# Kernel tuning notes

Measured on AMD Instinct MI355X. Metric: run time of the kernel, lower is better.

The kernel has to match this reference:

```python
import jax, jax.numpy as jnp
import numpy as np

DIM = 2048
NUM_HEADS = 16
NUM_KV_HEADS = 4
HEAD_DIM = DIM // NUM_HEADS  # 128


def apply_rotary_emb(x, freqs_cis):
    # x: [b, s, h, head_dim]; freqs_cis: [s, head_dim//2, 2]
    b, s, h, d = x.shape
    xs = x.reshape(b, s, h, d // 2, 2)
    fc = freqs_cis.reshape(1, s, 1, d // 2, 2)
    real = xs[..., 0] * fc[..., 0] - xs[..., 1] * fc[..., 1]
    imag = xs[..., 1] * fc[..., 0] + xs[..., 0] * fc[..., 1]
    return jnp.stack([real, imag], axis=-1).reshape(b, s, h, d)


def setup_inputs() -> dict:
    key = jax.random.key(0)
    k1, k2, k3, k4 = jax.random.split(key, 4)
    b, s = 2, 2048
    x = jax.random.normal(k1, (b, s, DIM), dtype=jnp.float32)
    freqs_cis = jax.random.uniform(k2, (s, HEAD_DIM // 2, 2), dtype=jnp.float32)
    total_kv_dim = (NUM_HEADS + 2 * NUM_KV_HEADS) * HEAD_DIM  # 3072
    wqkv = jax.random.normal(k3, (total_kv_dim, DIM), dtype=jnp.float32) * (DIM ** -0.5)
    wo = jax.random.normal(k4, (DIM, DIM), dtype=jnp.float32) * (DIM ** -0.5)
    return {"x": x, "freqs_cis": freqs_cis, "wqkv": wqkv, "wo": wo}


def reference(x, freqs_cis, wqkv, wo):
    b, s, _ = x.shape
    kv_size = NUM_KV_HEADS * HEAD_DIM
    qkv = jnp.einsum('bsd,od->bso', x, wqkv)
    xq = qkv[..., :DIM].reshape(b, s, NUM_HEADS, HEAD_DIM)
    xk = qkv[..., DIM:DIM + kv_size].reshape(b, s, NUM_KV_HEADS, HEAD_DIM)
    xv = qkv[..., DIM + kv_size:].reshape(b, s, NUM_KV_HEADS, HEAD_DIM)
    xq = apply_rotary_emb(xq, freqs_cis)
    xk = apply_rotary_emb(xk, freqs_cis)
    # -> [b, h, s, d]
    q = xq.transpose(0, 2, 1, 3)
    k = xk.transpose(0, 2, 1, 3)
    v = xv.transpose(0, 2, 1, 3)
    rep = NUM_HEADS // NUM_KV_HEADS
    k = jnp.repeat(k, rep, axis=1)
    v = jnp.repeat(v, rep, axis=1)
    scale = HEAD_DIM ** -0.5
    scores = jnp.einsum('bhqd,bhkd->bhqk', q, k) * scale
    causal = jnp.tril(jnp.ones((s, s), dtype=bool))
    scores = jnp.where(causal[None, None], scores, jnp.finfo(scores.dtype).min)
    attn = jax.nn.softmax(scores, axis=-1)
    out = jnp.einsum('bhqk,bhkd->bhqd', attn, v)
    out = out.transpose(0, 2, 1, 3).reshape(b, s, DIM)
    return jnp.einsum('bsd,od->bso', out, wo)
```

## Files before the change

kernel.cpp:

```cpp
#include <hip/hip_runtime.h>
#include <stdint.h>

typedef uint16_t u16;
typedef float f32x4 __attribute__((ext_vector_type(4)));
typedef short bf16x8 __attribute__((ext_vector_type(8)));

constexpr int NB = 2, NS = 2048, ND = 2048, NH = 16, NKVH = 4, HDIM = 128;
constexpr int QKVD = 3072;
constexpr int TOK = NB * NS;
constexpr float SM_SCALE = 0.08838834764831845f;
constexpr float LOG2E = 1.4426950408889634f;
constexpr float QK_SCALE = SM_SCALE * LOG2E;

#define WAITVM(N) asm volatile("s_waitcnt vmcnt(" #N ")" ::: "memory")
#define WAITLGKM0 asm volatile("s_waitcnt lgkmcnt(0)" ::: "memory")
#define MEMFENCE asm volatile("" ::: "memory")

__device__ __forceinline__ u16 f2bf(float f) {
  union { float f; uint32_t u; } v; v.f = f;
  return (u16)((v.u + 0x7fffu + ((v.u >> 16) & 1u)) >> 16);
}
__device__ __forceinline__ float bf2f(u16 h) {
  union { uint32_t u; float f; } v; v.u = ((uint32_t)h) << 16; return v.f;
}
__device__ __forceinline__ uint32_t cvt_pk_bf16(float lo, float hi) {
  uint32_t r;
  asm("v_cvt_pk_bf16_f32 %0, %1, %2" : "=v"(r) : "v"(lo), "v"(hi));
  return r;
}

__device__ __forceinline__ void gload_lds16(const void* g, void* l) {
  void* gv = const_cast<void*>(g);
  __builtin_amdgcn_global_load_lds(
      (__attribute__((address_space(1))) void*)gv,
      (__attribute__((address_space(3))) void*)l, 16, 0, 0);
}

__global__ __launch_bounds__(256) void cvt_bf16(const float* __restrict__ src,
                                                u16* __restrict__ dst, int n4) {
  int i = blockIdx.x * 256 + threadIdx.x;
  if (i >= n4) return;
  const float4 v = reinterpret_cast<const float4*>(src)[i];
  union { u16 h[4]; uint2 u; } o;
  o.h[0] = f2bf(v.x); o.h[1] = f2bf(v.y); o.h[2] = f2bf(v.z); o.h[3] = f2bf(v.w);
  reinterpret_cast<uint2*>(dst)[i] = o.u;
}

template <int OUTBF>
__global__ __launch_bounds__(256, 2)
void gemm_bt(const u16* __restrict__ A, const u16* __restrict__ Bm,
             void* __restrict__ Cv, int M, int N, int K) {
  __shared__ u16 As[2][128 * 32];
  __shared__ u16 Bs[2][128 * 32];
  const int tid = threadIdx.x;
  const int lane = tid & 63;
  const int wid = tid >> 6;
  const int wr = wid >> 1, wc = wid & 1;
  const int rowA0 = blockIdx.y * 128, colB0 = blockIdx.x * 128;
  const int lr = lane & 15;
  const int lk = (lane >> 4) * 8;
  const char* Ab = (const char*)A;
  const char* Bb = (const char*)Bm;
  f32x4 acc[4][4] = {};
  const int nkt = K >> 5;

  auto STAGE = [&](int kt, int buf) {
#pragma unroll
    for (int p = 0; p < 2; ++p) {
      int o = p * 4096 + tid * 16;
      int row = o >> 6, kb = o & 63;
      gload_lds16(Ab + ((size_t)(rowA0 + row) * K + kt * 32) * 2 + kb, (char*)As[buf] + o);
      gload_lds16(Bb + ((size_t)(colB0 + row) * K + kt * 32) * 2 + kb, (char*)Bs[buf] + o);
    }
  };

  STAGE(0, 0);
  for (int kt = 0; kt < nkt; ++kt) {
    const int cur = kt & 1;
    if (kt + 1 < nkt) { STAGE(kt + 1, cur ^ 1); WAITVM(4); }
    else              { WAITVM(0); }
    __builtin_amdgcn_s_barrier();
    MEMFENCE;
    const u16* Ac = As[cur];
    const u16* Bc = Bs[cur];
    bf16x8 af[4], bfr[4];
#pragma unroll
    for (int m = 0; m < 4; ++m)
      af[m] = *(const bf16x8*)&Ac[(wr * 64 + m * 16 + lr) * 32 + lk];
#pragma unroll
    for (int n = 0; n < 4; ++n)
      bfr[n] = *(const bf16x8*)&Bc[(wc * 64 + n * 16 + lr) * 32 + lk];
    __builtin_amdgcn_s_setprio(1);
#pragma unroll
    for (int m = 0; m < 4; ++m)
#pragma unroll
      for (int n = 0; n < 4; ++n)
        acc[m][n] = __builtin_amdgcn_mfma_f32_16x16x32_bf16(af[m], bfr[n], acc[m][n], 0, 0, 0);
    __builtin_amdgcn_s_setprio(0);
    WAITLGKM0;
    __builtin_amdgcn_s_barrier();
    MEMFENCE;
  }
#pragma unroll
  for (int m = 0; m < 4; ++m) {
    int row0 = rowA0 + wr * 64 + m * 16 + (lane >> 4) * 4;
#pragma unroll
    for (int n = 0; n < 4; ++n) {
      int col = colB0 + wc * 64 + n * 16 + lr;
#pragma unroll
      for (int r = 0; r < 4; ++r) {
        if (OUTBF)
          ((u16*)Cv)[(size_t)(row0 + r) * N + col] = f2bf(acc[m][n][r]);
        else
          ((float*)Cv)[(size_t)(row0 + r) * N + col] = acc[m][n][r];
      }
    }
  }
}

__global__ __launch_bounds__(256)
void rope_split(const u16* __restrict__ qkv, const float* __restrict__ fc,
                u16* __restrict__ Qb, u16* __restrict__ Kb, u16* __restrict__ Vt) {
  const int tok = blockIdx.x;
  const int b = tok >> 11, s = tok & 2047;
  const int tid = threadIdx.x;
  const u16* base = qkv + (size_t)tok * QKVD;
  for (int pp = tid; pp < 1024; pp += 256) {
    int h = pp >> 6, p = pp & 63;
    float x0 = bf2f(base[h * 128 + 2 * p]);
    float x1 = bf2f(base[h * 128 + 2 * p + 1]);
    float c = fc[(s * 64 + p) * 2];
    float sn = fc[(s * 64 + p) * 2 + 1];
    size_t o = ((size_t)(b * NH + h) * NS + s) * HDIM + 2 * p;
    Qb[o] = f2bf(x0 * c - x1 * sn);
    Qb[o + 1] = f2bf(x1 * c + x0 * sn);
  }
  for (int pp = tid; pp < 256; pp += 256) {
    int kv = pp >> 6, p = pp & 63;
    float x0 = bf2f(base[ND + kv * 128 + 2 * p]);
    float x1 = bf2f(base[ND + kv * 128 + 2 * p + 1]);
    float c = fc[(s * 64 + p) * 2];
    float sn = fc[(s * 64 + p) * 2 + 1];
    size_t o = ((size_t)(b * NKVH + kv) * NS + s) * HDIM + 2 * p;
    Kb[o] = f2bf((x0 * c - x1 * sn) * QK_SCALE);
    Kb[o + 1] = f2bf((x1 * c + x0 * sn) * QK_SCALE);
  }
  for (int i = tid; i < 512; i += 256) {
    int kv = i >> 7, d = i & 127;
    float v = bf2f(base[ND + NKVH * HDIM + kv * 128 + d]);
    Vt[((size_t)(b * NKVH + kv) * HDIM + d) * NS + s] = f2bf(v);
  }
}

__global__ __launch_bounds__(512, 2)
void flash_attn(const u16* __restrict__ Qb, const u16* __restrict__ Kb,
                const u16* __restrict__ Vt, u16* __restrict__ Ob) {
  __shared__ u16 Ks[2][64 * 128];
  __shared__ u16 Vs[2][128 * 64];
  const int idx = blockIdx.x;
  const int grp = idx & 7;
  const int b = grp >> 2, kvh = grp & 3;
  const int rest = idx >> 3;
  const int h = kvh * 4 + (rest & 3);
  const int qt = (NS / 128 - 1) - (rest >> 2);
  const int tid = threadIdx.x, lane = tid & 63, w = tid >> 6;
  const int lr = lane & 15, lg = lane >> 4;

  bf16x8 aq[4];
  {
    const u16* Qrow = Qb + ((size_t)(b * NH + h) * NS + qt * 128 + w * 16 + lr) * HDIM;
#pragma unroll
    for (int ks = 0; ks < 4; ++ks)
      aq[ks] = *(const bf16x8*)(Qrow + ks * 32 + lg * 8);
  }
  bf16x8 ones;
#pragma unroll
  for (int j = 0; j < 8; ++j) ones[j] = (short)0x3F80;

  float mrun = -1e30f;
  f32x4 accl = {0.f, 0.f, 0.f, 0.f};
  f32x4 acco[8] = {};

  const char* Kbase = (const char*)(Kb + (size_t)(b * NKVH + kvh) * NS * HDIM);
  const char* Vbase = (const char*)(Vt + (size_t)(b * NKVH + kvh) * HDIM * NS);
  const int qglob = qt * 128 + w * 16 + lr;
  const int qrow0 = qt * 128 + w * 16 + lg * 4;
  const int wave_min_row = qt * 128 + w * 16;
  const int wave_max_row = wave_min_row + 15;

  auto STAGE = [&](int kt, int buf) {
#pragma unroll
    for (int p = 0; p < 2; ++p) {
      int o = p * 8192 + tid * 16;
      int krow = o >> 8, kwb = o & 255;
      gload_lds16(Kbase + (size_t)(kt * 64 + krow) * 256 + (kwb ^ ((krow & 7) << 4)),
                  (char*)Ks[buf] + o);
      int vrow = o >> 7, vwb = o & 127;
      gload_lds16(Vbase + (size_t)vrow * (NS * 2) + kt * 128 + (vwb ^ ((vrow & 7) << 4)),
                  (char*)Vs[buf] + o);
    }
  };

  const int ktmax = 2 * qt + 1;
  STAGE(0, 0);
  for (int kt = 0; kt <= ktmax; ++kt) {
    const int cur = kt & 1;
    if (kt < ktmax) { STAGE(kt + 1, cur ^ 1); WAITVM(4); }
    else            { WAITVM(0); }
    __builtin_amdgcn_s_barrier();
    MEMFENCE;

    if (kt * 64 <= wave_max_row) {
      const char* Kc = (const char*)Ks[cur];
      const char* Vc = (const char*)Vs[cur];

      f32x4 accs[4] = {};
      __builtin_amdgcn_s_setprio(1);
#pragma unroll
      for (int n = 0; n < 4; ++n) {
        int row = n * 16 + lr;
        int swz = (row & 7) << 4;
#pragma unroll
        for (int ks = 0; ks < 4; ++ks) {
          int cb = (ks * 32 + lg * 8) * 2;
          bf16x8 bk = *(const bf16x8*)(Kc + row * 256 + (cb ^ swz));
          accs[n] = __builtin_amdgcn_mfma_f32_16x16x32_bf16(bk, aq[ks], accs[n], 0, 0, 0);
        }
      }
      __builtin_amdgcn_s_setprio(0);

      if (kt * 64 + 63 > wave_min_row) {
#pragma unroll
        for (int n = 0; n < 4; ++n) {
          int kbase = kt * 64 + n * 16 + lg * 4;
#pragma unroll
          for (int r = 0; r < 4; ++r)
            if (kbase + r > qglob) accs[n][r] = -1e30f;
        }
      }

      float pmax = fmaxf(fmaxf(fmaxf(accs[0][0], accs[0][1]), fmaxf(accs[0][2], accs[0][3])),
                         fmaxf(fmaxf(accs[1][0], accs[1][1]), fmaxf(accs[1][2], accs[1][3])));
      pmax = fmaxf(pmax,
             fmaxf(fmaxf(fmaxf(accs[2][0], accs[2][1]), fmaxf(accs[2][2], accs[2][3])),
                   fmaxf(fmaxf(accs[3][0], accs[3][1]), fmaxf(accs[3][2], accs[3][3]))));
      pmax = fmaxf(pmax, __shfl_xor(pmax, 16, 64));
      pmax = fmaxf(pmax, __shfl_xor(pmax, 32, 64));

      bool ok = (pmax <= mrun + 8.f);
      if (!__all(ok)) {
        float mnew = fmaxf(mrun, pmax);
        float alpha = exp2f(mrun - mnew);
        mrun = mnew;
        float alr[4];
#pragma unroll
        for (int r = 0; r < 4; ++r)
          alr[r] = __shfl(alpha, lg * 4 + r, 64);
#pragma unroll
        for (int r = 0; r < 4; ++r) accl[r] *= alr[r];
#pragma unroll
        for (int n2 = 0; n2 < 8; ++n2)
#pragma unroll
          for (int r = 0; r < 4; ++r) acco[n2][r] *= alr[r];
      }

      uint32_t w0[4], w1[4];
#pragma unroll
      for (int n = 0; n < 4; ++n) {
        float p0 = exp2f(accs[n][0] - mrun);
        float p1 = exp2f(accs[n][1] - mrun);
        float p2 = exp2f(accs[n][2] - mrun);
        float p3 = exp2f(accs[n][3] - mrun);
        w0[n] = cvt_pk_bf16(p0, p1);
        w1[n] = cvt_pk_bf16(p2, p3);
      }

      const int s1 = ((lg & 1) << 5) | lr;
      const int s2 = s1 + 16;
      uint32_t F[4][4];
#pragma unroll
      for (int n = 0; n < 4; ++n) {
        F[n][0] = __shfl((int)w0[n], s1, 64);
        F[n][1] = __shfl((int)w1[n], s1, 64);
        F[n][2] = __shfl((int)w0[n], s2, 64);
        F[n][3] = __shfl((int)w1[n], s2, 64);
      }
      const bool hi = (lg & 2);
      bf16x8 pa[2];
#pragma unroll
      for (int ks = 0; ks < 2; ++ks) {
        union { uint32_t d[4]; bf16x8 v; } u;
#pragma unroll
        for (int j = 0; j < 4; ++j)
          u.d[j] = hi ? F[ks * 2 + 1][j] : F[ks * 2][j];
        pa[ks] = u.v;
      }

      __builtin_amdgcn_s_setprio(1);
#pragma unroll
      for (int ks = 0; ks < 2; ++ks) {
        int cb = (ks * 32 + lg * 8) * 2;
#pragma unroll
        for (int n2 = 0; n2 < 8; ++n2) {
          int d = n2 * 16 + lr;
          bf16x8 bv = *(const bf16x8*)(Vc + d * 128 + (cb ^ ((d & 7) << 4)));
          acco[n2] = __builtin_amdgcn_mfma_f32_16x16x32_bf16(pa[ks], bv, acco[n2], 0, 0, 0);
        }
        accl = __builtin_amdgcn_mfma_f32_16x16x32_bf16(pa[ks], ones, accl, 0, 0, 0);
      }
      __builtin_amdgcn_s_setprio(0);
    }
    WAITLGKM0;
    __builtin_amdgcn_s_barrier();
    MEMFENCE;
  }

#pragma unroll
  for (int n2 = 0; n2 < 8; ++n2) {
    int d = n2 * 16 + lr;
#pragma unroll
    for (int r = 0; r < 4; ++r) {
      int q = qrow0 + r;
      Ob[((size_t)b * NS + q) * ND + h * HDIM + d] = f2bf(acco[n2][r] / accl[r]);
    }
  }
}

extern "C" void kernel_launch(void* const* d_in, const int* in_sizes, int n_in,
                              void* d_out, int out_size, void* d_ws, size_t ws_size,
                              hipStream_t stream) {
  const float* x = (const float*)d_in[0];
  const float* fc = (const float*)d_in[1];
  const float* wqkv = (const float*)d_in[2];
  const float* wo = (const float*)d_in[3];
  float* out = (float*)d_out;
  char* ws = (char*)d_ws;
  size_t off = 0;
  u16* xb = (u16*)(ws + off);    off += (size_t)TOK * ND * 2;
  u16* wqkvb = (u16*)(ws + off); off += (size_t)QKVD * ND * 2;
  u16* wob = (u16*)(ws + off);   off += (size_t)ND * ND * 2;
  u16* qkv = (u16*)(ws + off);   off += (size_t)TOK * QKVD * 2;
  u16* Qb = (u16*)(ws + off);    off += (size_t)NB * NH * NS * HDIM * 2;
  u16* Kb = (u16*)(ws + off);    off += (size_t)NB * NKVH * NS * HDIM * 2;
  u16* Vtb = (u16*)(ws + off);   off += (size_t)NB * NKVH * NS * HDIM * 2;
  u16* attnb = (u16*)(ws + off); off += (size_t)TOK * ND * 2;
  (void)ws_size; (void)in_sizes; (void)n_in; (void)out_size;

  cvt_bf16<<<TOK * ND / 4 / 256, 256, 0, stream>>>(x, xb, TOK * ND / 4);
  cvt_bf16<<<QKVD * ND / 4 / 256, 256, 0, stream>>>(wqkv, wqkvb, QKVD * ND / 4);
  cvt_bf16<<<ND * ND / 4 / 256, 256, 0, stream>>>(wo, wob, ND * ND / 4);
  gemm_bt<1><<<dim3(QKVD / 128, TOK / 128), 256, 0, stream>>>(xb, wqkvb, qkv, TOK, QKVD, ND);
  rope_split<<<TOK, 256, 0, stream>>>(qkv, fc, Qb, Kb, Vtb);
  flash_attn<<<dim3(NB * NKVH * (NH / NKVH) * (NS / 128)), 512, 0, stream>>>(Qb, Kb, Vtb, attnb);
  gemm_bt<0><<<dim3(ND / 128, TOK / 128), 256, 0, stream>>>(attnb, wob, out, TOK, ND, ND);
}
```

Baseline: 236.5 us.

## Deepen GEMM K-tile to 64 with XOR-swizzled LDS and staggered B prefetch

```diff
diff --git a/kernel.cpp b/kernel.cpp
--- a/kernel.cpp
+++ b/kernel.cpp
@@ -50,60 +50,99 @@
 __global__ __launch_bounds__(256, 2)
 void gemm_bt(const u16* __restrict__ A, const u16* __restrict__ Bm,
              void* __restrict__ Cv, int M, int N, int K) {
-  __shared__ u16 As[2][128 * 32];
-  __shared__ u16 Bs[2][128 * 32];
+  __shared__ u16 As[2][128 * 64];
+  __shared__ u16 Bs[2][128 * 64];
   const int tid = threadIdx.x;
   const int lane = tid & 63;
   const int wid = tid >> 6;
   const int wr = wid >> 1, wc = wid & 1;
   const int rowA0 = blockIdx.y * 128, colB0 = blockIdx.x * 128;
-  const int lr = lane & 15;
-  const int lk = (lane >> 4) * 8;
+  const int lr = lane & 15, lg = lane >> 4;
   const char* Ab = (const char*)A;
   const char* Bb = (const char*)Bm;
   f32x4 acc[4][4] = {};
-  const int nkt = K >> 5;
-
-  auto STAGE = [&](int kt, int buf) {
-#pragma unroll
-    for (int p = 0; p < 2; ++p) {
+  const int nkt = K >> 6;
+
+  auto SA = [&](int kt, int buf) {
+#pragma unroll
+    for (int p = 0; p < 4; ++p) {
       int o = p * 4096 + tid * 16;
-      int row = o >> 6, kb = o & 63;
-      gload_lds16(Ab + ((size_t)(rowA0 + row) * K + kt * 32) * 2 + kb, (char*)As[buf] + o);
-      gload_lds16(Bb + ((size_t)(colB0 + row) * K + kt * 32) * 2 + kb, (char*)Bs[buf] + o);
+      int row = o >> 7, cb = o & 127;
+      gload_lds16(Ab + ((size_t)(rowA0 + row) * K + kt * 64) * 2 + (cb ^ ((row & 7) << 4)),
+                  (char*)As[buf] + o);
     }
   };
-
-  STAGE(0, 0);
+  auto SB = [&](int kt, int buf) {
+#pragma unroll
+    for (int p = 0; p < 4; ++p) {
+      int o = p * 4096 + tid * 16;
+      int row = o >> 7, cb = o & 127;
+      gload_lds16(Bb + ((size_t)(colB0 + row) * K + kt * 64) * 2 + (cb ^ ((row & 7) << 4)),
+                  (char*)Bs[buf] + o);
+    }
+  };
+
+  SA(0, 0); SB(0, 0);
   for (int kt = 0; kt < nkt; ++kt) {
     const int cur = kt & 1;
-    if (kt + 1 < nkt) { STAGE(kt + 1, cur ^ 1); WAITVM(4); }
-    else              { WAITVM(0); }
+    const bool pf = (kt + 1 < nkt);
+    const char* Ac = (const char*)As[cur];
+    const char* Bc = (const char*)Bs[cur];
+
+    if (pf) { SA(kt + 1, cur ^ 1); WAITVM(4); } else { WAITVM(0); }
     __builtin_amdgcn_s_barrier();
     MEMFENCE;
-    const u16* Ac = As[cur];
-    const u16* Bc = Bs[cur];
-    bf16x8 af[4], bfr[4];
-#pragma unroll
-    for (int m = 0; m < 4; ++m)
-      af[m] = *(const bf16x8*)&Ac[(wr * 64 + m * 16 + lr) * 32 + lk];
-#pragma unroll
-    for (int n = 0; n < 4; ++n)
-      bfr[n] = *(const bf16x8*)&Bc[(wc * 64 + n * 16 + lr) * 32 + lk];
-    __builtin_amdgcn_s_setprio(1);
-#pragma unroll
-    for (int m = 0; m < 4; ++m)
-#pragma unroll
-      for (int n = 0; n < 4; ++n)
-        acc[m][n] = __builtin_amdgcn_mfma_f32_16x16x32_bf16(af[m], bfr[n], acc[m][n], 0, 0, 0);
-    __builtin_amdgcn_s_setprio(0);
-    WAITLGKM0;
+    bf16x8 af[4][2];
+#pragma unroll
+    for (int m = 0; m < 4; ++m) {
+      int row = wr * 64 + m * 16 + lr;
+      int sw = (row & 7) << 4;
+#pragma unroll
+      for (int ks = 0; ks < 2; ++ks)
+        af[m][ks] = *(const bf16x8*)(Ac + row * 128 + ((ks * 64 + lg * 16) ^ sw));
+    }
+    {
+      int row = wc * 64 + lr;
+      int sw = (row & 7) << 4;
+      bf16x8 b0 = *(const bf16x8*)(Bc + row * 128 + ((lg * 16) ^ sw));
+      bf16x8 b1 = *(const bf16x8*)(Bc + row * 128 + ((64 + lg * 16) ^ sw));
+      __builtin_amdgcn_s_setprio(1);
+#pragma unroll
+      for (int m = 0; m < 4; ++m)
+        acc[m][0] = __builtin_amdgcn_mfma_f32_16x16x32_bf16(af[m][0], b0, acc[m][0], 0, 0, 0);
+#pragma unroll
+      for (int m = 0; m < 4; ++m)
+        acc[m][0] = __builtin_amdgcn_mfma_f32_16x16x32_bf16(af[m][1], b1, acc[m][0], 0, 0, 0);
+      __builtin_amdgcn_s_setprio(0);
+    }
+    MEMFENCE;
     __builtin_amdgcn_s_barrier();
     MEMFENCE;
-  }
+
+#pragma unroll
+    for (int n = 1; n < 4; ++n) {
+      if (pf && n == 1) SB(kt + 1, cur ^ 1);
+      int row = wc * 64 + n * 16 + lr;
+      int sw = (row & 7) << 4;
+      bf16x8 b0 = *(const bf16x8*)(Bc + row * 128 + ((lg * 16) ^ sw));
+      bf16x8 b1 = *(const bf16x8*)(Bc + row * 128 + ((64 + lg * 16) ^ sw));
+      __builtin_amdgcn_s_setprio(1);
+#pragma unroll
+      for (int m = 0; m < 4; ++m)
+        acc[m][n] = __builtin_amdgcn_mfma_f32_16x16x32_bf16(af[m][0], b0, acc[m][n], 0, 0, 0);
+#pragma unroll
+      for (int m = 0; m < 4; ++m)
+        acc[m][n] = __builtin_amdgcn_mfma_f32_16x16x32_bf16(af[m][1], b1, acc[m][n], 0, 0, 0);
+      __builtin_amdgcn_s_setprio(0);
+      MEMFENCE;
+      __builtin_amdgcn_s_barrier();
+      MEMFENCE;
+    }
+  }
+
 #pragma unroll
   for (int m = 0; m < 4; ++m) {
-    int row0 = rowA0 + wr * 64 + m * 16 + (lane >> 4) * 4;
+    int row0 = rowA0 + wr * 64 + m * 16 + lg * 4;
 #pragma unroll
     for (int n = 0; n < 4; ++n) {
       int col = colB0 + wc * 64 + n * 16 + lr;
@@ -162,7 +201,8 @@
   const int b = grp >> 2, kvh = grp & 3;
   const int rest = idx >> 3;
   const int h = kvh * 4 + (rest & 3);
-  const int qt = (NS / 128 - 1) - (rest >> 2);
+  const int slot = rest >> 2;
+  const int qt = (slot < 8) ? (15 - slot) : (slot - 8);
   const int tid = threadIdx.x, lane = tid & 63, w = tid >> 6;
   const int lr = lane & 15, lg = lane >> 4;
 
```

Result: slower. 292.6 us (+23.7%).
